# Kernel tuning notes

Hardware: AMD Instinct MI355X
Metric: run time of the kernel (lower is better)

Reference implementation:

```python
import jax, jax.numpy as jnp
import numpy as np


def setup_inputs() -> dict:
    key = jax.random.key(0)
    k1, k2, k3 = jax.random.split(key, 3)
    B, N, D, YD = 128, 500000, 64, 1
    return {
        "x": jax.random.normal(k1, (B, D), dtype=jnp.float32),
        "pool_x": jax.random.normal(k2, (N, D), dtype=jnp.float32),
        "pool_y": jax.random.normal(k3, (N, YD), dtype=jnp.float32),
        "size_retrieval_set": 10,
    }


def reference(x, pool_x, pool_y, size_retrieval_set):
    # Euclidean cdist via the expanded quadratic form (same math as torch.cdist p=2).
    x_sq = jnp.sum(x * x, axis=-1, keepdims=True)            # [B, 1]
    p_sq = jnp.sum(pool_x * pool_x, axis=-1)                 # [N]
    cross = jnp.einsum("bd,nd->bn", x, pool_x)               # [B, N]
    dist = jnp.sqrt(jnp.maximum(x_sq + p_sq[None, :] - 2.0 * cross, 0.0))  # [B, N]
    # ascending sort + take first k  ==  top_k of negated distances
    _, indices = jax.lax.top_k(-dist, size_retrieval_set)    # [B, k]
    # gather + concat: [B, k, x_dim + y_dim]
    retrieval_set = jnp.concatenate([pool_x[indices], pool_y[indices]], axis=-1)
    return retrieval_set
```

## Files before the change

### kernel.cpp

```cpp
#include <hip/hip_runtime.h>
#include <hip/hip_bf16.h>
#include <cfloat>
#include <climits>

typedef short  short8v __attribute__((ext_vector_type(8)));
typedef float  f32x4   __attribute__((ext_vector_type(4)));

#define NQ    128
#define SR    16
#define SPW   8
#define RPC   (SR * SPW)
#define EMIT  3
#define K2    6
#define KSEL  24
#define KK    10

__device__ __forceinline__ bool pair_less(float d1, int i1, float d2, int i2) {
    return (d1 < d2) || (d1 == d2 && i1 < i2);
}

__device__ __forceinline__ unsigned pk2(float a, float b) {
    union { __hip_bfloat162 h; unsigned u; } cv;
    cv.h = __float22bfloat162_rn(make_float2(a, b));
    return cv.u;
}
__device__ __forceinline__ short8v pack8(float4 a, float4 b) {
    union { unsigned u[4]; short8v s; } cv;
    cv.u[0] = pk2(a.x, a.y); cv.u[1] = pk2(a.z, a.w);
    cv.u[2] = pk2(b.x, b.y); cv.u[3] = pk2(b.z, b.w);
    return cv.s;
}

__device__ __forceinline__ void ins2(float (&d)[2], int (&ix)[2], float key, int idx) {
    if (!(key < d[1])) return;
    d[1] = key; ix[1] = idx;
    bool sw = d[1] < d[0];
    float a = d[0], b = d[1]; int ai = ix[0], bi2 = ix[1];
    d[0] = sw ? b : a; ix[0] = sw ? bi2 : ai;
    d[1] = sw ? a : b; ix[1] = sw ? ai : bi2;
}

__device__ __forceinline__ void ins3p(float (&d)[3], int (&ix)[3], float key, int idx) {
    if (!pair_less(key, idx, d[2], ix[2])) return;
    d[2] = key; ix[2] = idx;
#pragma unroll
    for (int j = 2; j > 0; --j) {
        float a = d[j - 1], b = d[j]; int ai = ix[j - 1], bi2 = ix[j];
        bool sw = pair_less(b, bi2, a, ai);
        d[j - 1] = sw ? b : a; ix[j - 1] = sw ? bi2 : ai;
        d[j]     = sw ? a : b; ix[j]     = sw ? ai : bi2;
    }
}

__device__ __forceinline__ void ins6(float (&d)[K2], int (&ix)[K2], float key, int idx) {
    if (!pair_less(key, idx, d[K2 - 1], ix[K2 - 1])) return;
    d[K2 - 1] = key; ix[K2 - 1] = idx;
#pragma unroll
    for (int j = K2 - 1; j > 0; --j) {
        float a = d[j - 1], b = d[j]; int ai = ix[j - 1], bi2 = ix[j];
        bool sw = pair_less(b, bi2, a, ai);
        d[j - 1] = sw ? b : a; ix[j - 1] = sw ? bi2 : ai;
        d[j]     = sw ? a : b; ix[j]     = sw ? ai : bi2;
    }
}

__device__ __forceinline__ void argmin64(float& k, int& i, int& l) {
#pragma unroll
    for (int off = 32; off; off >>= 1) {
        float ok = __shfl_xor(k, off);
        int   oi = __shfl_xor(i, off);
        int   ol = __shfl_xor(l, off);
        bool take = pair_less(ok, oi, k, i) || (ok == k && oi == i && ol < l);
        k = take ? ok : k; i = take ? oi : i; l = take ? ol : l;
    }
}

__global__ __launch_bounds__(256, 4) void phase1(
        const float* __restrict__ x, const float* __restrict__ pool_x,
        float2* __restrict__ cand, int N, int nchunks) {
    const int t = threadIdx.x, wv = t >> 6, lane = t & 63;
    const int c = lane & 15, g = lane >> 4;
    const int qbase = (wv >> 1) * 64;
    const int chunk = blockIdx.x * 2 + (wv & 1);
    const long brow = (long)chunk * RPC;

    short8v bfrag[4][2];
#pragma unroll
    for (int tt = 0; tt < 4; ++tt)
#pragma unroll
        for (int ks = 0; ks < 2; ++ks) {
            const float* xp = x + (qbase + tt * 16 + c) * 64 + ks * 32 + g * 8;
            float4 u0 = *(const float4*)xp;
            float4 u1 = *(const float4*)(xp + 4);
            u0.x *= -2.f; u0.y *= -2.f; u0.z *= -2.f; u0.w *= -2.f;
            u1.x *= -2.f; u1.y *= -2.f; u1.z *= -2.f; u1.w *= -2.f;
            bfrag[tt][ks] = pack8(u0, u1);
        }

    short8v b2 = {0, 0, 0, 0, 0, 0, 0, 0};
    b2[0] = (short)0x3F80;

    float bd[4][2]; int bi[4][2];
#pragma unroll
    for (int tt = 0; tt < 4; ++tt) {
        bd[tt][0] = FLT_MAX; bd[tt][1] = FLT_MAX;
        bi[tt][0] = INT_MAX; bi[tt][1] = INT_MAX;
    }

    float4 buf[2][4];
    auto LOAD = [&](int s, int b) {
        long r = brow + (long)s * SR + c;
        if (r > (long)N - 1) r = (long)N - 1;
        const float* pr = pool_x + r * 64 + g * 8;
        buf[b][0] = *(const float4*)pr;
        buf[b][1] = *(const float4*)(pr + 4);
        buf[b][2] = *(const float4*)(pr + 32);
        buf[b][3] = *(const float4*)(pr + 36);
    };
    LOAD(0, 0);

#pragma unroll
    for (int s = 0; s < SPW; ++s) {
        const int b = s & 1;
        if (s + 1 < SPW) LOAD(s + 1, b ^ 1);
        float4 f0 = buf[b][0], f1 = buf[b][1], f2 = buf[b][2], f3 = buf[b][3];

        float ps = f0.x * f0.x + f0.y * f0.y + f0.z * f0.z + f0.w * f0.w
                 + f1.x * f1.x + f1.y * f1.y + f1.z * f1.z + f1.w * f1.w
                 + f2.x * f2.x + f2.y * f2.y + f2.z * f2.z + f2.w * f2.w
                 + f3.x * f3.x + f3.y * f3.y + f3.z * f3.z + f3.w * f3.w;
        if (brow + (long)s * SR + c >= N) ps = __builtin_inff();

        short8v a2 = {0, 0, 0, 0, 0, 0, 0, 0};
        union { unsigned u; short s2[2]; } pv; pv.u = pk2(ps, 0.f);
        a2[0] = pv.s2[0];

        short8v a0 = pack8(f0, f1);
        short8v a1 = pack8(f2, f3);

        f32x4 zc = {0.f, 0.f, 0.f, 0.f};
        f32x4 pacc = __builtin_amdgcn_mfma_f32_16x16x32_bf16(a2, b2, zc, 0, 0, 0);

        const int rowb = (int)brow + s * SR + g * 4;
#pragma unroll
        for (int tt = 0; tt < 4; ++tt) {
            f32x4 acc = __builtin_amdgcn_mfma_f32_16x16x32_bf16(a0, bfrag[tt][0], pacc, 0, 0, 0);
            acc = __builtin_amdgcn_mfma_f32_16x16x32_bf16(a1, bfrag[tt][1], acc, 0, 0, 0);
            float mn = fminf(fminf(acc[0], acc[1]), fminf(acc[2], acc[3]));
            if (mn < bd[tt][1]) {
#pragma unroll
                for (int r = 0; r < 4; ++r) ins2(bd[tt], bi[tt], acc[r], rowb + r);
            }
        }
    }

#pragma unroll
    for (int tt = 0; tt < 4; ++tt) {
        float md[3] = {bd[tt][0], bd[tt][1], FLT_MAX};
        int   mi[3] = {bi[tt][0], bi[tt][1], INT_MAX};
#pragma unroll
        for (int m = 16; m <= 32; m <<= 1) {
            float od[3]; int oi[3];
#pragma unroll
            for (int j = 0; j < 3; ++j) { od[j] = __shfl_xor(md[j], m); oi[j] = __shfl_xor(mi[j], m); }
#pragma unroll
            for (int j = 0; j < 3; ++j) ins3p(md, mi, od[j], oi[j]);
        }
        if (g < 3) {
            int q = qbase + tt * 16 + c;
            cand[((size_t)chunk * NQ + q) * EMIT + g] =
                make_float2(md[g], __int_as_float(mi[g]));
        }
    }
}

__global__ __launch_bounds__(256) void phase2(
        const float2* __restrict__ cand, const float* __restrict__ x,
        const float* __restrict__ pool_x, const float* __restrict__ pool_y,
        float* __restrict__ out, int nchunks, int N) {
    __shared__ float xs[64];
    __shared__ float wd[4 * KSEL]; __shared__ int wi[4 * KSEL];
    __shared__ float sd[KSEL];     __shared__ int si[KSEL];
    __shared__ float rk[64];
    __shared__ int   fi[KK];

    const int t = threadIdx.x, wave = t >> 6, lane = t & 63;
    const int q = blockIdx.x;
    if (t < 64) xs[t] = x[q * 64 + t];

    float d[K2]; int ix[K2];
#pragma unroll
    for (int j = 0; j < K2; ++j) { d[j] = FLT_MAX; ix[j] = INT_MAX; }

    for (int ch = t; ch < nchunks; ch += 256) {
        const float2* e = cand + ((size_t)ch * NQ + q) * EMIT;
#pragma unroll
        for (int g2 = 0; g2 < EMIT; ++g2) {
            float2 v = e[g2];
            ins6(d, ix, v.x, __float_as_int(v.y));
        }
    }

    for (int r = 0; r < KSEL; ++r) {
        float mk = d[0]; int mi = ix[0]; int ml = lane;
        argmin64(mk, mi, ml);
        if (lane == ml) {
#pragma unroll
            for (int j = 0; j < K2 - 1; ++j) { d[j] = d[j + 1]; ix[j] = ix[j + 1]; }
            d[K2 - 1] = FLT_MAX; ix[K2 - 1] = INT_MAX;
        }
        if (lane == 0) { wd[wave * KSEL + r] = mk; wi[wave * KSEL + r] = mi; }
    }
    __syncthreads();

    if (wave == 0) {
        float e0 = wd[lane]; int e0i = wi[lane];
        float e1 = (lane + 64 < 4 * KSEL) ? wd[lane + 64] : FLT_MAX;
        int  e1i = (lane + 64 < 4 * KSEL) ? wi[lane + 64] : INT_MAX;
        if (pair_less(e1, e1i, e0, e0i)) {
            float tf = e0; e0 = e1; e1 = tf;
            int   ti = e0i; e0i = e1i; e1i = ti;
        }
        for (int r = 0; r < KSEL; ++r) {
            float mk = e0; int mi = e0i; int ml = lane;
            argmin64(mk, mi, ml);
            if (lane == ml) { e0 = e1; e0i = e1i; e1 = FLT_MAX; e1i = INT_MAX; }
            if (lane == 0) { sd[r] = mk; si[r] = mi; }
        }
    }
    __syncthreads();

    if (t < 64) {
        float key = FLT_MAX;
        if (t < KSEL) {
            int idx = si[t];
            if (idx >= 0 && idx < N) {
                const float4* pr = (const float4*)(pool_x + (size_t)idx * 64);
                const float4* xv = (const float4*)xs;
                float psq = 0.f, dot = 0.f;
#pragma unroll
                for (int k4 = 0; k4 < 16; ++k4) {
                    float4 p = pr[k4]; float4 xw = xv[k4];
                    psq += p.x * p.x + p.y * p.y + p.z * p.z + p.w * p.w;
                    dot += p.x * xw.x + p.y * xw.y + p.z * xw.z + p.w * xw.w;
                }
                key = psq - 2.0f * dot;
            }
        }
        rk[t] = key;
    }
    __syncthreads();

    if (wave == 0) {
        float mykey = rk[lane];
        int myidx = (lane < KSEL) ? si[lane] : INT_MAX;
        for (int r = 0; r < KK; ++r) {
            float mk = mykey; int mi = myidx; int ml = lane;
            argmin64(mk, mi, ml);
            if (lane == ml) { mykey = FLT_MAX; myidx = INT_MAX; }
            if (lane == 0) fi[r] = mi;
        }
    }
    __syncthreads();

    for (int e = t; e < KK * 65; e += 256) {
        int j = e / 65, cdim = e - j * 65;
        int idx = fi[j];
        out[(size_t)q * (KK * 65) + e] = (cdim < 64) ? pool_x[(size_t)idx * 64 + cdim]
                                                     : pool_y[idx];
    }
}

extern "C" void kernel_launch(void* const* d_in, const int* in_sizes, int n_in,
                              void* d_out, int out_size, void* d_ws, size_t ws_size,
                              hipStream_t stream) {
    const float* x      = (const float*)d_in[0];
    const float* pool_x = (const float*)d_in[1];
    const float* pool_y = (const float*)d_in[2];
    const int N = in_sizes[1] / 64;

    const int nblocks = (N + 2 * RPC - 1) / (2 * RPC);
    const int nchunks = nblocks * 2;

    float2* cand = (float2*)d_ws;

    hipLaunchKernelGGL(phase1, dim3(nblocks), dim3(256), 0, stream,
                       x, pool_x, cand, N, nchunks);
    hipLaunchKernelGGL(phase2, dim3(NQ), dim3(256), 0, stream,
                       cand, x, pool_x, pool_y, (float*)d_out, nchunks, N);
}
```

Before: 258.1 us.

## Make phase1 a persistent grid-stride kernel with cross-chunk prefetch

Phase1 now launches a fixed grid of 1024 blocks. Each wave walks chunks with a stride of 2048 instead of getting one chunk per launch slot. The last step of each chunk prefetches the first rows of the wave's next chunk, so the load pipeline stays busy across chunk boundaries. This amortizes the per-wave setup (loading and packing the query fragments) over several chunks and cuts block launch overhead. The trade-off is more register pressure and a fixed grid size that may not match the device's occupancy.

```diff
diff --git a/kernel.cpp b/kernel.cpp
--- a/kernel.cpp
+++ b/kernel.cpp
@@ -8,9 +8,11 @@
 
 #define NQ    128
 #define SR    16
-#define SPW   8
-#define RPC   (SR * SPW)
+#define SPC   8
+#define RPC   (SR * SPC)
 #define EMIT  3
+#define GBLK  1024
+#define CSTR  2048
 #define K2    6
 #define KSEL  24
 #define KK    10
@@ -81,8 +83,7 @@
     const int t = threadIdx.x, wv = t >> 6, lane = t & 63;
     const int c = lane & 15, g = lane >> 4;
     const int qbase = (wv >> 1) * 64;
-    const int chunk = blockIdx.x * 2 + (wv & 1);
-    const long brow = (long)chunk * RPC;
+    const int c0 = blockIdx.x * 2 + (wv & 1);
 
     short8v bfrag[4][2];
 #pragma unroll
@@ -100,16 +101,9 @@
     short8v b2 = {0, 0, 0, 0, 0, 0, 0, 0};
     b2[0] = (short)0x3F80;
 
-    float bd[4][2]; int bi[4][2];
-#pragma unroll
-    for (int tt = 0; tt < 4; ++tt) {
-        bd[tt][0] = FLT_MAX; bd[tt][1] = FLT_MAX;
-        bi[tt][0] = INT_MAX; bi[tt][1] = INT_MAX;
-    }
-
     float4 buf[2][4];
-    auto LOAD = [&](int s, int b) {
-        long r = brow + (long)s * SR + c;
+    auto LOAD = [&](long rowbase, int b) {
+        long r = rowbase + c;
         if (r > (long)N - 1) r = (long)N - 1;
         const float* pr = pool_x + r * 64 + g * 8;
         buf[b][0] = *(const float4*)pr;
@@ -117,59 +111,76 @@
         buf[b][2] = *(const float4*)(pr + 32);
         buf[b][3] = *(const float4*)(pr + 36);
     };
-    LOAD(0, 0);
-
-#pragma unroll
-    for (int s = 0; s < SPW; ++s) {
-        const int b = s & 1;
-        if (s + 1 < SPW) LOAD(s + 1, b ^ 1);
-        float4 f0 = buf[b][0], f1 = buf[b][1], f2 = buf[b][2], f3 = buf[b][3];
-
-        float ps = f0.x * f0.x + f0.y * f0.y + f0.z * f0.z + f0.w * f0.w
-                 + f1.x * f1.x + f1.y * f1.y + f1.z * f1.z + f1.w * f1.w
-                 + f2.x * f2.x + f2.y * f2.y + f2.z * f2.z + f2.w * f2.w
-                 + f3.x * f3.x + f3.y * f3.y + f3.z * f3.z + f3.w * f3.w;
-        if (brow + (long)s * SR + c >= N) ps = __builtin_inff();
-
-        short8v a2 = {0, 0, 0, 0, 0, 0, 0, 0};
-        union { unsigned u; short s2[2]; } pv; pv.u = pk2(ps, 0.f);
-        a2[0] = pv.s2[0];
-
-        short8v a0 = pack8(f0, f1);
-        short8v a1 = pack8(f2, f3);
-
-        f32x4 zc = {0.f, 0.f, 0.f, 0.f};
-        f32x4 pacc = __builtin_amdgcn_mfma_f32_16x16x32_bf16(a2, b2, zc, 0, 0, 0);
-
-        const int rowb = (int)brow + s * SR + g * 4;
+
+    if (c0 < nchunks) LOAD((long)c0 * RPC, 0);
+
+#pragma unroll 1
+    for (int cc = c0; cc < nchunks; cc += CSTR) {
+        const long brow = (long)cc * RPC;
+
+        float bd[4][2]; int bi[4][2];
 #pragma unroll
         for (int tt = 0; tt < 4; ++tt) {
-            f32x4 acc = __builtin_amdgcn_mfma_f32_16x16x32_bf16(a0, bfrag[tt][0], pacc, 0, 0, 0);
-            acc = __builtin_amdgcn_mfma_f32_16x16x32_bf16(a1, bfrag[tt][1], acc, 0, 0, 0);
-            float mn = fminf(fminf(acc[0], acc[1]), fminf(acc[2], acc[3]));
-            if (mn < bd[tt][1]) {
-#pragma unroll
-                for (int r = 0; r < 4; ++r) ins2(bd[tt], bi[tt], acc[r], rowb + r);
-            }
-        }
-    }
-
-#pragma unroll
-    for (int tt = 0; tt < 4; ++tt) {
-        float md[3] = {bd[tt][0], bd[tt][1], FLT_MAX};
-        int   mi[3] = {bi[tt][0], bi[tt][1], INT_MAX};
-#pragma unroll
-        for (int m = 16; m <= 32; m <<= 1) {
-            float od[3]; int oi[3];
-#pragma unroll
-            for (int j = 0; j < 3; ++j) { od[j] = __shfl_xor(md[j], m); oi[j] = __shfl_xor(mi[j], m); }
-#pragma unroll
-            for (int j = 0; j < 3; ++j) ins3p(md, mi, od[j], oi[j]);
-        }
-        if (g < 3) {
-            int q = qbase + tt * 16 + c;
-            cand[((size_t)chunk * NQ + q) * EMIT + g] =
-                make_float2(md[g], __int_as_float(mi[g]));
+            bd[tt][0] = FLT_MAX; bd[tt][1] = FLT_MAX;
+            bi[tt][0] = INT_MAX; bi[tt][1] = INT_MAX;
+        }
+
+#pragma unroll
+        for (int s = 0; s < SPC; ++s) {
+            const int b = s & 1;
+            if (s + 1 < SPC) {
+                LOAD(brow + (long)(s + 1) * SR, b ^ 1);
+            } else if (cc + CSTR < nchunks) {
+                LOAD((long)(cc + CSTR) * RPC, b ^ 1);
+            }
+            float4 f0 = buf[b][0], f1 = buf[b][1], f2 = buf[b][2], f3 = buf[b][3];
+
+            float ps = f0.x * f0.x + f0.y * f0.y + f0.z * f0.z + f0.w * f0.w
+                     + f1.x * f1.x + f1.y * f1.y + f1.z * f1.z + f1.w * f1.w
+                     + f2.x * f2.x + f2.y * f2.y + f2.z * f2.z + f2.w * f2.w
+                     + f3.x * f3.x + f3.y * f3.y + f3.z * f3.z + f3.w * f3.w;
+            if (brow + (long)s * SR + c >= N) ps = __builtin_inff();
+
+            short8v a2 = {0, 0, 0, 0, 0, 0, 0, 0};
+            union { unsigned u; short s2[2]; } pv; pv.u = pk2(ps, 0.f);
+            a2[0] = pv.s2[0];
+
+            short8v a0 = pack8(f0, f1);
+            short8v a1 = pack8(f2, f3);
+
+            f32x4 zc = {0.f, 0.f, 0.f, 0.f};
+            f32x4 pacc = __builtin_amdgcn_mfma_f32_16x16x32_bf16(a2, b2, zc, 0, 0, 0);
+
+            const int rowb = (int)brow + s * SR + g * 4;
+#pragma unroll
+            for (int tt = 0; tt < 4; ++tt) {
+                f32x4 acc = __builtin_amdgcn_mfma_f32_16x16x32_bf16(a0, bfrag[tt][0], pacc, 0, 0, 0);
+                acc = __builtin_amdgcn_mfma_f32_16x16x32_bf16(a1, bfrag[tt][1], acc, 0, 0, 0);
+                float mn = fminf(fminf(acc[0], acc[1]), fminf(acc[2], acc[3]));
+                if (mn < bd[tt][1]) {
+#pragma unroll
+                    for (int r = 0; r < 4; ++r) ins2(bd[tt], bi[tt], acc[r], rowb + r);
+                }
+            }
+        }
+
+#pragma unroll
+        for (int tt = 0; tt < 4; ++tt) {
+            float md[3] = {bd[tt][0], bd[tt][1], FLT_MAX};
+            int   mi[3] = {bi[tt][0], bi[tt][1], INT_MAX};
+#pragma unroll
+            for (int m = 16; m <= 32; m <<= 1) {
+                float od[3]; int oi[3];
+#pragma unroll
+                for (int j = 0; j < 3; ++j) { od[j] = __shfl_xor(md[j], m); oi[j] = __shfl_xor(mi[j], m); }
+#pragma unroll
+                for (int j = 0; j < 3; ++j) ins3p(md, mi, od[j], oi[j]);
+            }
+            if (g < 3) {
+                int q = qbase + tt * 16 + c;
+                cand[((size_t)cc * NQ + q) * EMIT + g] =
+                    make_float2(md[g], __int_as_float(mi[g]));
+            }
         }
     }
 }
@@ -279,12 +290,11 @@
     const float* pool_y = (const float*)d_in[2];
     const int N = in_sizes[1] / 64;
 
-    const int nblocks = (N + 2 * RPC - 1) / (2 * RPC);
-    const int nchunks = nblocks * 2;
+    const int nchunks = (N + RPC - 1) / RPC;
 
     float2* cand = (float2*)d_ws;
 
-    hipLaunchKernelGGL(phase1, dim3(nblocks), dim3(256), 0, stream,
+    hipLaunchKernelGGL(phase1, dim3(GBLK), dim3(256), 0, stream,
                        x, pool_x, cand, N, nchunks);
     hipLaunchKernelGGL(phase2, dim3(NQ), dim3(256), 0, stream,
                        cand, x, pool_x, pool_y, (float*)d_out, nchunks, N);
```

After: 261.7 us. Within noise of the previous version (+1.4%).
